# Kernel tuning notes

Hardware: AMD Instinct MI355X
Metric: run time of the kernel (lower is better)

Reference implementation:

```python
import jax, jax.numpy as jnp
import numpy as np

B, L, DIM, H = 2, 2048, 1024, 16
HD = DIM // H  # head dim = 64
MASK_SCALE = -10 * 6  # faithful to the original source: mask_expand *= -10 * 6


def setup_inputs() -> dict:
    key = jax.random.key(0)
    ks = jax.random.split(key, 8)
    s = 1.0 / np.sqrt(DIM)
    return {
        "x": jax.random.normal(ks[0], (B, L, DIM), jnp.float32),
        "attention_mask": jax.random.uniform(ks[1], (B, L, L), jnp.float32),
        "Wq": jax.random.normal(ks[2], (DIM, DIM), jnp.float32) * s,
        "bq": jnp.zeros((DIM,), jnp.float32),
        "Wk": jax.random.normal(ks[3], (DIM, DIM), jnp.float32) * s,
        "bk": jnp.zeros((DIM,), jnp.float32),
        "Wv": jax.random.normal(ks[4], (DIM, DIM), jnp.float32) * s,
        "bv": jnp.zeros((DIM,), jnp.float32),
    }


def _split_heads(t):
    # [B, L, DIM] -> [B, H, L, HD]
    return t.reshape(B, L, H, HD).transpose(0, 2, 1, 3)


def reference(x, attention_mask, Wq, bq, Wk, bk, Wv, bv):
    q = _split_heads(x @ Wq + bq)
    k = _split_heads(x @ Wk + bk)
    v = _split_heads(x @ Wv + bv)
    scale = float(HD) ** -0.5
    # full [B, H, L, L] score matrix, as in the original
    scores = jnp.einsum("bhqd,bhkd->bhqk", q, k) * scale
    scores = scores + attention_mask[:, None, :, :] * MASK_SCALE
    probs = jax.nn.softmax(scores, axis=-1)
    ctx = jnp.einsum("bhqk,bhkd->bhqd", probs, v)
    # merge heads back: [B, L, DIM]
    return ctx.transpose(0, 2, 1, 3).reshape(B, L, DIM)
```

## Files before the change

### kernel.cpp

```cpp
#include <hip/hip_runtime.h>

#define LL 2048
#define NHEADS 16
#define HDIM 64
#define QSCALE 0.18033688011112042f
#define MASKC1 -86.56170245333780f

typedef __attribute__((ext_vector_type(8))) __bf16 bf16x8;
typedef __attribute__((ext_vector_type(4))) float f32x4;

__device__ __forceinline__ unsigned short f2bf(float f) {
  unsigned int u = __builtin_bit_cast(unsigned int, f);
  u += 0x7fffu + ((u >> 16) & 1u);
  return (unsigned short)(u >> 16);
}

__device__ __forceinline__ bf16x8 ld_frag(const unsigned short* p) {
  return *reinterpret_cast<const bf16x8*>(p);
}

__device__ __forceinline__ void async_cp16(const unsigned short* g, unsigned short* l) {
  __builtin_amdgcn_global_load_lds(
      (const __attribute__((address_space(1))) unsigned int*)(unsigned long long)(g),
      (__attribute__((address_space(3))) unsigned int*)(unsigned int)(unsigned long long)(l),
      16, 0, 0);
}

__global__ __launch_bounds__(256) void cvt_x_kernel(const float* __restrict__ x,
                                                    unsigned short* __restrict__ xb) {
  int i = (blockIdx.x * 256 + threadIdx.x) * 4;
  float4 v = *reinterpret_cast<const float4*>(x + i);
  ushort4 o;
  o.x = f2bf(v.x); o.y = f2bf(v.y); o.z = f2bf(v.z); o.w = f2bf(v.w);
  *reinterpret_cast<ushort4*>(xb + i) = o;
}

__global__ __launch_bounds__(256) void transpose_w_kernel(const float* __restrict__ Wq,
                                                          const float* __restrict__ Wk,
                                                          const float* __restrict__ Wv,
                                                          unsigned short* __restrict__ WtAll) {
  int z = blockIdx.z;
  const float* W = (z == 0) ? Wq : (z == 1) ? Wk : Wv;
  unsigned short* dst = WtAll + (size_t)z * 1024 * 1024;
  int n0 = blockIdx.x * 64, k0 = blockIdx.y * 64;
  __shared__ float t[64][65];
  int tx = threadIdx.x & 63, ty = threadIdx.x >> 6;
#pragma unroll
  for (int p = 0; p < 16; ++p) {
    int kr = p * 4 + ty;
    t[kr][tx] = W[(size_t)(k0 + kr) * 1024 + n0 + tx];
  }
  __syncthreads();
#pragma unroll
  for (int p = 0; p < 16; ++p) {
    int nr = p * 4 + ty;
    dst[(size_t)(n0 + nr) * 1024 + k0 + tx] = f2bf(t[tx][nr]);
  }
}

__global__ __launch_bounds__(256) void em_prep_kernel(const float* __restrict__ mask,
                                                      unsigned short* __restrict__ em) {
  int row = blockIdx.y;
  int t = blockIdx.x * 256 + threadIdx.x;
  int kb = t >> 4, c = t & 15;
  const float* src = mask + (size_t)row * LL + kb * 64 + c;
  ushort4 o;
  o.x = f2bf(__builtin_amdgcn_exp2f(src[0]  * MASKC1));
  o.y = f2bf(__builtin_amdgcn_exp2f(src[16] * MASKC1));
  o.z = f2bf(__builtin_amdgcn_exp2f(src[32] * MASKC1));
  o.w = f2bf(__builtin_amdgcn_exp2f(src[48] * MASKC1));
  *reinterpret_cast<ushort4*>(em + (size_t)row * LL + kb * 64 + 4 * c) = o;
}

__global__ __launch_bounds__(256) void qkv_gemm_kernel(
    const unsigned short* __restrict__ xb, const unsigned short* __restrict__ WtAll,
    const float* __restrict__ bq, const float* __restrict__ bk, const float* __restrict__ bv,
    unsigned short* __restrict__ qkv) {
  const int z = blockIdx.z;
  const unsigned short* Wt = WtAll + (size_t)z * 1024 * 1024;
  const float* bias = (z == 0) ? bq : (z == 1) ? bk : bv;
  unsigned short* outb = qkv + (size_t)z * 4194304;

  __shared__ __align__(16) unsigned short smem[16384];
  unsigned short* As = smem;
  unsigned short* Bs = smem + 8192;

  const int tid = threadIdx.x;
  const int w = tid >> 6, lane = tid & 63, g = lane >> 4, cc = lane & 15;
  const int wm = w >> 1, wn = w & 1;
  const int m0 = blockIdx.y * 128, n0 = blockIdx.x * 128;
  const int srow = lane >> 3;
  const int gc = ((lane & 7) - srow) & 7;
  const unsigned short* ga = xb + (size_t)(m0 + w * 32 + srow) * 1024 + gc * 8;
  const unsigned short* gb = Wt + (size_t)(n0 + w * 32 + srow) * 1024 + gc * 8;
  unsigned short* la = As + w * 2048;
  unsigned short* lb = Bs + w * 2048;

  f32x4 acc[4][4];
#pragma unroll
  for (int i = 0; i < 4; ++i)
#pragma unroll
    for (int j = 0; j < 4; ++j) acc[i][j] = (f32x4)0.0f;

  for (int kk = 0; kk < 1024; kk += 64) {
    __syncthreads();
#pragma unroll
    for (int i = 0; i < 4; ++i) {
      async_cp16(ga + i * 8192 + kk, la + i * 512);
      async_cp16(gb + i * 8192 + kk, lb + i * 512);
    }
    __syncthreads();
    bf16x8 af[4][2], bfr[4][2];
#pragma unroll
    for (int mt = 0; mt < 4; ++mt)
#pragma unroll
      for (int ks = 0; ks < 2; ++ks)
        af[mt][ks] = ld_frag(&As[(wm * 64 + mt * 16 + cc) * 64 + ((4 * ks + g + cc) & 7) * 8]);
#pragma unroll
    for (int nt = 0; nt < 4; ++nt)
#pragma unroll
      for (int ks = 0; ks < 2; ++ks)
        bfr[nt][ks] = ld_frag(&Bs[(wn * 64 + nt * 16 + cc) * 64 + ((4 * ks + g + cc) & 7) * 8]);
#pragma unroll
    for (int mt = 0; mt < 4; ++mt)
#pragma unroll
      for (int nt = 0; nt < 4; ++nt)
#pragma unroll
        for (int ks = 0; ks < 2; ++ks)
          acc[mt][nt] = __builtin_amdgcn_mfma_f32_16x16x32_bf16(af[mt][ks], bfr[nt][ks],
                                                                acc[mt][nt], 0, 0, 0);
  }

  if (z != 2) {
    const float sc = (z == 0) ? QSCALE : 1.0f;
#pragma unroll
    for (int nt = 0; nt < 4; ++nt) {
      int n = n0 + wn * 64 + nt * 16 + cc;
      float bval = bias[n];
      int h = n >> 6, d = n & 63;
#pragma unroll
      for (int mt = 0; mt < 4; ++mt) {
#pragma unroll
        for (int r = 0; r < 4; ++r) {
          int m = m0 + wm * 64 + mt * 16 + g * 4 + r;
          int b = m >> 11, l = m & 2047;
          outb[(((size_t)(b * NHEADS + h) * LL) + l) * HDIM + d] =
              f2bf((acc[mt][nt][r] + bval) * sc);
        }
      }
    }
  } else {
    __syncthreads();
#pragma unroll
    for (int nt = 0; nt < 4; ++nt) {
      int nr = wn * 64 + nt * 16 + cc;
      float bval = bias[n0 + nr];
#pragma unroll
      for (int mt = 0; mt < 4; ++mt)
#pragma unroll
        for (int r = 0; r < 4; ++r)
          smem[nr * 128 + wm * 64 + 16 * g + 4 * r + mt] = f2bf(acc[mt][nt][r] + bval);
    }
    __syncthreads();
    int row = tid >> 1, half = tid & 1;
    int n = n0 + row, hh = n >> 6, dd = n & 63;
    int bb = m0 >> 11, l0 = (m0 & 2047) + half * 64;
    unsigned short* dst = outb + ((size_t)(bb * NHEADS + hh) * HDIM + dd) * LL + l0;
#pragma unroll
    for (int i = 0; i < 8; ++i)
      *reinterpret_cast<uint4*>(dst + i * 8) =
          *reinterpret_cast<const uint4*>(&smem[row * 128 + half * 64 + i * 8]);
  }
}

__global__ __launch_bounds__(256) void flash_kernel(
    const unsigned short* __restrict__ Qb, const unsigned short* __restrict__ Kb,
    const unsigned short* __restrict__ Vt, const unsigned short* __restrict__ Em,
    float* __restrict__ out) {
  const int bh = blockIdx.y, b = bh >> 4, h = bh & 15;
  const int q0 = blockIdx.x * 128;
  const int tid = threadIdx.x, w = tid >> 6, lane = tid & 63, g = lane >> 4, cc = lane & 15;
  const size_t bhoff = (size_t)bh * LL * HDIM;

  __shared__ __align__(16) unsigned short Ps[128 * 72];
  __shared__ __align__(16) unsigned short Ks[2][64 * 64];
  __shared__ __align__(16) unsigned short Vs[2][64 * 64];

  bf16x8 aq[2][2];
#pragma unroll
  for (int mt = 0; mt < 2; ++mt)
#pragma unroll
    for (int ks = 0; ks < 2; ++ks)
      aq[mt][ks] = *reinterpret_cast<const bf16x8*>(
          Qb + bhoff + (size_t)(q0 + w * 32 + mt * 16 + cc) * HDIM + ks * 32 + g * 8);

  const int srow = lane >> 3;
  const int gcs = ((lane & 7) - srow) & 7;
  const unsigned short* kg0 = Kb + bhoff + (size_t)(w * 8 + srow) * HDIM + gcs * 8;
  const unsigned short* kg1 = Kb + bhoff + (size_t)(32 + w * 8 + srow) * HDIM + gcs * 8;
  const unsigned short* vg0 = Vt + bhoff + (size_t)(w * 8 + srow) * LL + gcs * 8;
  const unsigned short* vg1 = Vt + bhoff + (size_t)(32 + w * 8 + srow) * LL + gcs * 8;

  float li[2][4];
  f32x4 oacc[2][4];
#pragma unroll
  for (int mt = 0; mt < 2; ++mt) {
#pragma unroll
    for (int r = 0; r < 4; ++r) li[mt][r] = 0.0f;
#pragma unroll
    for (int nt = 0; nt < 4; ++nt) oacc[mt][nt] = (f32x4)0.0f;
  }

  const unsigned short* embase = Em + ((size_t)b * LL + q0 + w * 32) * LL + 4 * cc;

  {
    async_cp16(kg0, Ks[0] + w * 512);
    async_cp16(kg1, Ks[0] + (w + 4) * 512);
    async_cp16(vg0, Vs[0] + w * 512);
    async_cp16(vg1, Vs[0] + (w + 4) * 512);
  }

  for (int kt = 0; kt < 32; ++kt) {
    const int buf = kt & 1;
    __syncthreads();
    if (kt + 1 < 32) {
      const int nb = buf ^ 1;
      async_cp16(kg0 + (size_t)(kt + 1) * 64 * HDIM, Ks[nb] + w * 512);
      async_cp16(kg1 + (size_t)(kt + 1) * 64 * HDIM, Ks[nb] + (w + 4) * 512);
      async_cp16(vg0 + (kt + 1) * 64, Vs[nb] + w * 512);
      async_cp16(vg1 + (kt + 1) * 64, Vs[nb] + (w + 4) * 512);
    }
    uint2 emv[2][4];
#pragma unroll
    for (int mt = 0; mt < 2; ++mt)
#pragma unroll
      for (int r = 0; r < 4; ++r)
        emv[mt][r] = *reinterpret_cast<const uint2*>(
            embase + (size_t)(mt * 16 + g * 4 + r) * LL + kt * 64);

    bf16x8 bk_[4][2];
#pragma unroll
    for (int nt = 0; nt < 4; ++nt)
#pragma unroll
      for (int ks = 0; ks < 2; ++ks)
        bk_[nt][ks] =
            ld_frag(&Ks[buf][(nt * 16 + cc) * 64 + ((4 * ks + g + cc) & 7) * 8]);
    f32x4 sacc[2][4];
#pragma unroll
    for (int mt = 0; mt < 2; ++mt)
#pragma unroll
      for (int nt = 0; nt < 4; ++nt) sacc[mt][nt] = (f32x4)0.0f;
#pragma unroll
    for (int mt = 0; mt < 2; ++mt)
#pragma unroll
      for (int nt = 0; nt < 4; ++nt)
#pragma unroll
        for (int ks = 0; ks < 2; ++ks)
          sacc[mt][nt] = __builtin_amdgcn_mfma_f32_16x16x32_bf16(aq[mt][ks], bk_[nt][ks],
                                                                 sacc[mt][nt], 0, 0, 0);

#pragma unroll
    for (int mt = 0; mt < 2; ++mt) {
#pragma unroll
      for (int r = 0; r < 4; ++r) {
        unsigned int ex = emv[mt][r].x, ey = emv[mt][r].y;
        float e0 = __builtin_bit_cast(float, ex << 16);
        float e1 = __builtin_bit_cast(float, ex & 0xffff0000u);
        float e2 = __builtin_bit_cast(float, ey << 16);
        float e3 = __builtin_bit_cast(float, ey & 0xffff0000u);
        float p0 = __builtin_amdgcn_exp2f(sacc[mt][0][r]) * e0;
        float p1 = __builtin_amdgcn_exp2f(sacc[mt][1][r]) * e1;
        float p2 = __builtin_amdgcn_exp2f(sacc[mt][2][r]) * e2;
        float p3 = __builtin_amdgcn_exp2f(sacc[mt][3][r]) * e3;
        unsigned int u01 = __builtin_amdgcn_perm(__builtin_bit_cast(unsigned int, p1),
                                                 __builtin_bit_cast(unsigned int, p0),
                                                 0x07060302u);
        unsigned int u23 = __builtin_amdgcn_perm(__builtin_bit_cast(unsigned int, p3),
                                                 __builtin_bit_cast(unsigned int, p2),
                                                 0x07060302u);
        li[mt][r] += __builtin_bit_cast(float, u01 << 16) +
                     __builtin_bit_cast(float, u01 & 0xffff0000u) +
                     __builtin_bit_cast(float, u23 << 16) +
                     __builtin_bit_cast(float, u23 & 0xffff0000u);
        uint2 pk; pk.x = u01; pk.y = u23;
        *reinterpret_cast<uint2*>(&Ps[(w * 32 + mt * 16 + g * 4 + r) * 72 + 4 * cc]) = pk;
      }
    }
    asm volatile("" ::: "memory");

    bf16x8 ap[2][2], bv[4][2];
#pragma unroll
    for (int mt = 0; mt < 2; ++mt)
#pragma unroll
      for (int ks = 0; ks < 2; ++ks)
        ap[mt][ks] = ld_frag(&Ps[(w * 32 + mt * 16 + cc) * 72 + ks * 32 + g * 8]);
#pragma unroll
    for (int nt = 0; nt < 4; ++nt)
#pragma unroll
      for (int ks = 0; ks < 2; ++ks)
        bv[nt][ks] =
            ld_frag(&Vs[buf][(nt * 16 + cc) * 64 + ((4 * ks + g + cc) & 7) * 8]);
#pragma unroll
    for (int mt = 0; mt < 2; ++mt)
#pragma unroll
      for (int nt = 0; nt < 4; ++nt)
#pragma unroll
        for (int ks = 0; ks < 2; ++ks)
          oacc[mt][nt] = __builtin_amdgcn_mfma_f32_16x16x32_bf16(ap[mt][ks], bv[nt][ks],
                                                                 oacc[mt][nt], 0, 0, 0);
  }

#pragma unroll
  for (int mt = 0; mt < 2; ++mt)
#pragma unroll
    for (int r = 0; r < 4; ++r) {
      float s = li[mt][r];
      s += __shfl_xor(s, 1);
      s += __shfl_xor(s, 2);
      s += __shfl_xor(s, 4);
      s += __shfl_xor(s, 8);
      float inv = 1.0f / s;
      int qrow = q0 + w * 32 + mt * 16 + g * 4 + r;
#pragma unroll
      for (int nt = 0; nt < 4; ++nt)
        out[((size_t)b * LL + qrow) * 1024 + h * 64 + nt * 16 + cc] = oacc[mt][nt][r] * inv;
    }
}

extern "C" void kernel_launch(void* const* d_in, const int* in_sizes, int n_in,
                              void* d_out, int out_size, void* d_ws, size_t ws_size,
                              hipStream_t stream) {
  const float* x    = (const float*)d_in[0];
  const float* mask = (const float*)d_in[1];
  const float* Wq   = (const float*)d_in[2];
  const float* bq   = (const float*)d_in[3];
  const float* Wk   = (const float*)d_in[4];
  const float* bk   = (const float*)d_in[5];
  const float* Wv   = (const float*)d_in[6];
  const float* bv   = (const float*)d_in[7];
  float* out = (float*)d_out;
  (void)in_sizes; (void)n_in; (void)out_size; (void)ws_size;

  char* ws = (char*)d_ws;
  unsigned short* qkv = (unsigned short*)(ws);
  unsigned short* xb  = (unsigned short*)(ws + (24u << 20));
  unsigned short* Wt  = (unsigned short*)(ws + (32u << 20));
  unsigned short* em  = (unsigned short*)(ws + (24u << 20));

  cvt_x_kernel<<<dim3(4096), dim3(256), 0, stream>>>(x, xb);
  transpose_w_kernel<<<dim3(16, 16, 3), dim3(256), 0, stream>>>(Wq, Wk, Wv, Wt);
  qkv_gemm_kernel<<<dim3(8, 32, 3), dim3(256), 0, stream>>>(xb, Wt, bq, bk, bv, qkv);
  em_prep_kernel<<<dim3(2, 4096), dim3(256), 0, stream>>>(mask, em);
  flash_kernel<<<dim3(16, 32), dim3(256), 0, stream>>>(qkv, qkv + 4194304, qkv + 8388608,
                                                       em, out);
}
```

Measured before the change: 215.9 us.

## Pre-tile log-mask in MFMA fragment layout and seed score accumulators with it

The mask prep now stores the scaled mask in bf16 in log space, laid out per block and thread to match the MFMA accumulator fragment. The flash kernel loads it with two contiguous 16-byte loads and uses it as the initial score accumulator, which removes the per-element multiply by exp(mask). Query tiles shrink from 128 to 64 rows, giving twice as many blocks with a launch-bounds occupancy hint and a remapped block order that groups work for L2 locality. The P tile in LDS now uses an XOR swizzle instead of padding. Rounding the scaled log-mask to bf16 before the exp changes numerics and may add error for large mask values.

```diff
diff --git a/kernel.cpp b/kernel.cpp
--- a/kernel.cpp
+++ b/kernel.cpp
@@ -58,18 +58,26 @@
   }
 }
 
-__global__ __launch_bounds__(256) void em_prep_kernel(const float* __restrict__ mask,
-                                                      unsigned short* __restrict__ em) {
-  int row = blockIdx.y;
-  int t = blockIdx.x * 256 + threadIdx.x;
-  int kb = t >> 4, c = t & 15;
-  const float* src = mask + (size_t)row * LL + kb * 64 + c;
-  ushort4 o;
-  o.x = f2bf(__builtin_amdgcn_exp2f(src[0]  * MASKC1));
-  o.y = f2bf(__builtin_amdgcn_exp2f(src[16] * MASKC1));
-  o.z = f2bf(__builtin_amdgcn_exp2f(src[32] * MASKC1));
-  o.w = f2bf(__builtin_amdgcn_exp2f(src[48] * MASKC1));
-  *reinterpret_cast<ushort4*>(em + (size_t)row * LL + kb * 64 + 4 * c) = o;
+__global__ __launch_bounds__(256) void lem_prep_kernel(const float* __restrict__ mask,
+                                                       unsigned short* __restrict__ lem) {
+  const int qb = blockIdx.x, kt = blockIdx.y, b = blockIdx.z;
+  const int tid = threadIdx.x;
+  const int w = tid >> 6, lane = tid & 63, g = lane >> 4, cc = lane & 15;
+  const float* src = mask + ((size_t)b * LL + qb * 64 + w * 16 + g * 4) * LL + kt * 64 + cc;
+  unsigned int u[8];
+#pragma unroll
+  for (int nt = 0; nt < 4; ++nt) {
+    unsigned short h0 = f2bf(src[0 * LL + nt * 16] * MASKC1);
+    unsigned short h1 = f2bf(src[1 * LL + nt * 16] * MASKC1);
+    unsigned short h2 = f2bf(src[2 * LL + nt * 16] * MASKC1);
+    unsigned short h3 = f2bf(src[3 * LL + nt * 16] * MASKC1);
+    u[nt * 2]     = (unsigned int)h0 | ((unsigned int)h1 << 16);
+    u[nt * 2 + 1] = (unsigned int)h2 | ((unsigned int)h3 << 16);
+  }
+  uint4* dst = reinterpret_cast<uint4*>(
+      lem + ((((size_t)b * 32 + qb) * 32 + kt) * 256 + tid) * 16);
+  dst[0] = make_uint4(u[0], u[1], u[2], u[3]);
+  dst[1] = make_uint4(u[4], u[5], u[6], u[7]);
 }
 
 __global__ __launch_bounds__(256) void qkv_gemm_kernel(
@@ -173,26 +181,27 @@
   }
 }
 
-__global__ __launch_bounds__(256) void flash_kernel(
+__global__ __launch_bounds__(256, 4) void flash_kernel(
     const unsigned short* __restrict__ Qb, const unsigned short* __restrict__ Kb,
-    const unsigned short* __restrict__ Vt, const unsigned short* __restrict__ Em,
+    const unsigned short* __restrict__ Vt, const unsigned short* __restrict__ Lem,
     float* __restrict__ out) {
-  const int bh = blockIdx.y, b = bh >> 4, h = bh & 15;
-  const int q0 = blockIdx.x * 128;
+  const int id = blockIdx.y * 32 + blockIdx.x;
+  const int nid = (id & 7) * 128 + (id >> 3);
+  const int qb = nid & 31, bh = nid >> 5;
+  const int b = bh >> 4, h = bh & 15;
+  const int q0 = qb * 64;
   const int tid = threadIdx.x, w = tid >> 6, lane = tid & 63, g = lane >> 4, cc = lane & 15;
   const size_t bhoff = (size_t)bh * LL * HDIM;
 
-  __shared__ __align__(16) unsigned short Ps[128 * 72];
+  __shared__ __align__(16) unsigned short Ps[64 * 64];
   __shared__ __align__(16) unsigned short Ks[2][64 * 64];
   __shared__ __align__(16) unsigned short Vs[2][64 * 64];
 
-  bf16x8 aq[2][2];
-#pragma unroll
-  for (int mt = 0; mt < 2; ++mt)
-#pragma unroll
-    for (int ks = 0; ks < 2; ++ks)
-      aq[mt][ks] = *reinterpret_cast<const bf16x8*>(
-          Qb + bhoff + (size_t)(q0 + w * 32 + mt * 16 + cc) * HDIM + ks * 32 + g * 8);
+  bf16x8 aq[2];
+#pragma unroll
+  for (int ks = 0; ks < 2; ++ks)
+    aq[ks] = *reinterpret_cast<const bf16x8*>(
+        Qb + bhoff + (size_t)(q0 + w * 16 + cc) * HDIM + ks * 32 + g * 8);
 
   const int srow = lane >> 3;
   const int gcs = ((lane & 7) - srow) & 7;
@@ -201,17 +210,15 @@
   const unsigned short* vg0 = Vt + bhoff + (size_t)(w * 8 + srow) * LL + gcs * 8;
   const unsigned short* vg1 = Vt + bhoff + (size_t)(32 + w * 8 + srow) * LL + gcs * 8;
 
-  float li[2][4];
-  f32x4 oacc[2][4];
-#pragma unroll
-  for (int mt = 0; mt < 2; ++mt) {
-#pragma unroll
-    for (int r = 0; r < 4; ++r) li[mt][r] = 0.0f;
-#pragma unroll
-    for (int nt = 0; nt < 4; ++nt) oacc[mt][nt] = (f32x4)0.0f;
-  }
-
-  const unsigned short* embase = Em + ((size_t)b * LL + q0 + w * 32) * LL + 4 * cc;
+  const uint4* lemp = reinterpret_cast<const uint4*>(
+      Lem + ((((size_t)b * 32 + qb) * 32 + 0) * 256 + tid) * 16);
+
+  float li[4];
+  f32x4 oacc[4];
+#pragma unroll
+  for (int r = 0; r < 4; ++r) li[r] = 0.0f;
+#pragma unroll
+  for (int nt = 0; nt < 4; ++nt) oacc[nt] = (f32x4)0.0f;
 
   {
     async_cp16(kg0, Ks[0] + w * 512);
@@ -230,13 +237,32 @@
       async_cp16(vg0 + (kt + 1) * 64, Vs[nb] + w * 512);
       async_cp16(vg1 + (kt + 1) * 64, Vs[nb] + (w + 4) * 512);
     }
-    uint2 emv[2][4];
-#pragma unroll
-    for (int mt = 0; mt < 2; ++mt)
-#pragma unroll
-      for (int r = 0; r < 4; ++r)
-        emv[mt][r] = *reinterpret_cast<const uint2*>(
-            embase + (size_t)(mt * 16 + g * 4 + r) * LL + kt * 64);
+    uint4 e0 = lemp[0], e1 = lemp[1];
+    lemp += 512;
+    f32x4 sacc[4];
+    {
+      unsigned int ux, uy;
+      ux = e0.x; uy = e0.y;
+      sacc[0][0] = __builtin_bit_cast(float, ux << 16);
+      sacc[0][1] = __builtin_bit_cast(float, ux & 0xffff0000u);
+      sacc[0][2] = __builtin_bit_cast(float, uy << 16);
+      sacc[0][3] = __builtin_bit_cast(float, uy & 0xffff0000u);
+      ux = e0.z; uy = e0.w;
+      sacc[1][0] = __builtin_bit_cast(float, ux << 16);
+      sacc[1][1] = __builtin_bit_cast(float, ux & 0xffff0000u);
+      sacc[1][2] = __builtin_bit_cast(float, uy << 16);
+      sacc[1][3] = __builtin_bit_cast(float, uy & 0xffff0000u);
+      ux = e1.x; uy = e1.y;
+      sacc[2][0] = __builtin_bit_cast(float, ux << 16);
+      sacc[2][1] = __builtin_bit_cast(float, ux & 0xffff0000u);
+      sacc[2][2] = __builtin_bit_cast(float, uy << 16);
+      sacc[2][3] = __builtin_bit_cast(float, uy & 0xffff0000u);
+      ux = e1.z; uy = e1.w;
+      sacc[3][0] = __builtin_bit_cast(float, ux << 16);
+      sacc[3][1] = __builtin_bit_cast(float, ux & 0xffff0000u);
+      sacc[3][2] = __builtin_bit_cast(float, uy << 16);
+      sacc[3][3] = __builtin_bit_cast(float, uy & 0xffff0000u);
+    }
 
     bf16x8 bk_[4][2];
 #pragma unroll
@@ -245,55 +271,40 @@
       for (int ks = 0; ks < 2; ++ks)
         bk_[nt][ks] =
             ld_frag(&Ks[buf][(nt * 16 + cc) * 64 + ((4 * ks + g + cc) & 7) * 8]);
-    f32x4 sacc[2][4];
-#pragma unroll
-    for (int mt = 0; mt < 2; ++mt)
-#pragma unroll
-      for (int nt = 0; nt < 4; ++nt) sacc[mt][nt] = (f32x4)0.0f;
-#pragma unroll
-    for (int mt = 0; mt < 2; ++mt)
-#pragma unroll
-      for (int nt = 0; nt < 4; ++nt)
-#pragma unroll
-        for (int ks = 0; ks < 2; ++ks)
-          sacc[mt][nt] = __builtin_amdgcn_mfma_f32_16x16x32_bf16(aq[mt][ks], bk_[nt][ks],
-                                                                 sacc[mt][nt], 0, 0, 0);
-
-#pragma unroll
-    for (int mt = 0; mt < 2; ++mt) {
-#pragma unroll
-      for (int r = 0; r < 4; ++r) {
-        unsigned int ex = emv[mt][r].x, ey = emv[mt][r].y;
-        float e0 = __builtin_bit_cast(float, ex << 16);
-        float e1 = __builtin_bit_cast(float, ex & 0xffff0000u);
-        float e2 = __builtin_bit_cast(float, ey << 16);
-        float e3 = __builtin_bit_cast(float, ey & 0xffff0000u);
-        float p0 = __builtin_amdgcn_exp2f(sacc[mt][0][r]) * e0;
-        float p1 = __builtin_amdgcn_exp2f(sacc[mt][1][r]) * e1;
-        float p2 = __builtin_amdgcn_exp2f(sacc[mt][2][r]) * e2;
-        float p3 = __builtin_amdgcn_exp2f(sacc[mt][3][r]) * e3;
-        unsigned int u01 = __builtin_amdgcn_perm(__builtin_bit_cast(unsigned int, p1),
-                                                 __builtin_bit_cast(unsigned int, p0),
-                                                 0x07060302u);
-        unsigned int u23 = __builtin_amdgcn_perm(__builtin_bit_cast(unsigned int, p3),
-                                                 __builtin_bit_cast(unsigned int, p2),
-                                                 0x07060302u);
-        li[mt][r] += __builtin_bit_cast(float, u01 << 16) +
-                     __builtin_bit_cast(float, u01 & 0xffff0000u) +
-                     __builtin_bit_cast(float, u23 << 16) +
-                     __builtin_bit_cast(float, u23 & 0xffff0000u);
-        uint2 pk; pk.x = u01; pk.y = u23;
-        *reinterpret_cast<uint2*>(&Ps[(w * 32 + mt * 16 + g * 4 + r) * 72 + 4 * cc]) = pk;
-      }
+#pragma unroll
+    for (int nt = 0; nt < 4; ++nt)
+#pragma unroll
+      for (int ks = 0; ks < 2; ++ks)
+        sacc[nt] = __builtin_amdgcn_mfma_f32_16x16x32_bf16(aq[ks], bk_[nt][ks],
+                                                           sacc[nt], 0, 0, 0);
+
+#pragma unroll
+    for (int r = 0; r < 4; ++r) {
+      float p0 = __builtin_amdgcn_exp2f(sacc[0][r]);
+      float p1 = __builtin_amdgcn_exp2f(sacc[1][r]);
+      float p2 = __builtin_amdgcn_exp2f(sacc[2][r]);
+      float p3 = __builtin_amdgcn_exp2f(sacc[3][r]);
+      unsigned int u01 = __builtin_amdgcn_perm(__builtin_bit_cast(unsigned int, p1),
+                                               __builtin_bit_cast(unsigned int, p0),
+                                               0x07060302u);
+      unsigned int u23 = __builtin_amdgcn_perm(__builtin_bit_cast(unsigned int, p3),
+                                               __builtin_bit_cast(unsigned int, p2),
+                                               0x07060302u);
+      li[r] += __builtin_bit_cast(float, u01 << 16) +
+               __builtin_bit_cast(float, u01 & 0xffff0000u) +
+               __builtin_bit_cast(float, u23 << 16) +
+               __builtin_bit_cast(float, u23 & 0xffff0000u);
+      const int row = w * 16 + g * 4 + r;
+      const int sidx = row * 64 + (((cc >> 1) ^ (row & 7)) << 3) + ((cc & 1) << 2);
+      uint2 pk; pk.x = u01; pk.y = u23;
+      *reinterpret_cast<uint2*>(&Ps[sidx]) = pk;
     }
     asm volatile("" ::: "memory");
 
-    bf16x8 ap[2][2], bv[4][2];
-#pragma unroll
-    for (int mt = 0; mt < 2; ++mt)
-#pragma unroll
-      for (int ks = 0; ks < 2; ++ks)
-        ap[mt][ks] = ld_frag(&Ps[(w * 32 + mt * 16 + cc) * 72 + ks * 32 + g * 8]);
+    bf16x8 ap[2], bv[4][2];
+#pragma unroll
+    for (int ks = 0; ks < 2; ++ks)
+      ap[ks] = ld_frag(&Ps[(w * 16 + cc) * 64 + (((ks * 4 + g) ^ (cc & 7)) << 3)]);
 #pragma unroll
     for (int nt = 0; nt < 4; ++nt)
 #pragma unroll
@@ -301,30 +312,26 @@
         bv[nt][ks] =
             ld_frag(&Vs[buf][(nt * 16 + cc) * 64 + ((4 * ks + g + cc) & 7) * 8]);
 #pragma unroll
-    for (int mt = 0; mt < 2; ++mt)
-#pragma unroll
-      for (int nt = 0; nt < 4; ++nt)
-#pragma unroll
-        for (int ks = 0; ks < 2; ++ks)
-          oacc[mt][nt] = __builtin_amdgcn_mfma_f32_16x16x32_bf16(ap[mt][ks], bv[nt][ks],
-                                                                 oacc[mt][nt], 0, 0, 0);
-  }
-
-#pragma unroll
-  for (int mt = 0; mt < 2; ++mt)
-#pragma unroll
-    for (int r = 0; r < 4; ++r) {
-      float s = li[mt][r];
-      s += __shfl_xor(s, 1);
-      s += __shfl_xor(s, 2);
-      s += __shfl_xor(s, 4);
-      s += __shfl_xor(s, 8);
-      float inv = 1.0f / s;
-      int qrow = q0 + w * 32 + mt * 16 + g * 4 + r;
-#pragma unroll
-      for (int nt = 0; nt < 4; ++nt)
-        out[((size_t)b * LL + qrow) * 1024 + h * 64 + nt * 16 + cc] = oacc[mt][nt][r] * inv;
-    }
+    for (int nt = 0; nt < 4; ++nt)
+#pragma unroll
+      for (int ks = 0; ks < 2; ++ks)
+        oacc[nt] = __builtin_amdgcn_mfma_f32_16x16x32_bf16(ap[ks], bv[nt][ks],
+                                                           oacc[nt], 0, 0, 0);
+  }
+
+#pragma unroll
+  for (int r = 0; r < 4; ++r) {
+    float s = li[r];
+    s += __shfl_xor(s, 1);
+    s += __shfl_xor(s, 2);
+    s += __shfl_xor(s, 4);
+    s += __shfl_xor(s, 8);
+    float inv = 1.0f / s;
+    int qrow = q0 + w * 16 + g * 4 + r;
+#pragma unroll
+    for (int nt = 0; nt < 4; ++nt)
+      out[((size_t)b * LL + qrow) * 1024 + h * 64 + nt * 16 + cc] = oacc[nt][r] * inv;
+  }
 }
 
 extern "C" void kernel_launch(void* const* d_in, const int* in_sizes, int n_in,
@@ -345,12 +352,12 @@
   unsigned short* qkv = (unsigned short*)(ws);
   unsigned short* xb  = (unsigned short*)(ws + (24u << 20));
   unsigned short* Wt  = (unsigned short*)(ws + (32u << 20));
-  unsigned short* em  = (unsigned short*)(ws + (24u << 20));
+  unsigned short* lem = (unsigned short*)(ws + (24u << 20));
 
   cvt_x_kernel<<<dim3(4096), dim3(256), 0, stream>>>(x, xb);
   transpose_w_kernel<<<dim3(16, 16, 3), dim3(256), 0, stream>>>(Wq, Wk, Wv, Wt);
   qkv_gemm_kernel<<<dim3(8, 32, 3), dim3(256), 0, stream>>>(xb, Wt, bq, bk, bv, qkv);
-  em_prep_kernel<<<dim3(2, 4096), dim3(256), 0, stream>>>(mask, em);
-  flash_kernel<<<dim3(16, 32), dim3(256), 0, stream>>>(qkv, qkv + 4194304, qkv + 8388608,
-                                                       em, out);
-}
+  lem_prep_kernel<<<dim3(32, 32, 2), dim3(256), 0, stream>>>(mask, lem);
+  flash_kernel<<<dim3(32, 32), dim3(256), 0, stream>>>(qkv, qkv + 4194304, qkv + 8388608,
+                                                       lem, out);
+}
```

Measured after the change: 219.6 us. Within noise of the previous version (+1.7%).

## Fold log-mask into MFMA accumulator init and keep P in registers

Applied to the files above, without the earlier changes.

The mask prep kernel now writes the scaled log-mask (not exp of it) in a per-thread fragment-ordered layout, so the flash kernel loads it with contiguous uint4 reads and uses it as the initial value of the score accumulator. The QK^T MFMA is computed transposed (K as A operand), so the exponentiated probabilities land directly in the register layout needed as the A operand of the PV MFMA. That removes the LDS round-trip for P and the per-element mask multiply. The V-transpose store layout in the QKV GEMM is permuted to match the new P key ordering. Blocks are also remapped across heads and occupancy is hinted at two blocks per SIMD; bf16 rounding of the log-mask and a larger prep layout are the trade-offs.

```diff
diff --git a/kernel.cpp b/kernel.cpp
--- a/kernel.cpp
+++ b/kernel.cpp
@@ -8,6 +8,7 @@
 
 typedef __attribute__((ext_vector_type(8))) __bf16 bf16x8;
 typedef __attribute__((ext_vector_type(4))) float f32x4;
+typedef __attribute__((ext_vector_type(4))) unsigned int u32x4;
 
 __device__ __forceinline__ unsigned short f2bf(float f) {
   unsigned int u = __builtin_bit_cast(unsigned int, f);
@@ -17,6 +18,17 @@
 
 __device__ __forceinline__ bf16x8 ld_frag(const unsigned short* p) {
   return *reinterpret_cast<const bf16x8*>(p);
+}
+
+__device__ __forceinline__ float bflo(unsigned int u) {
+  return __builtin_bit_cast(float, u << 16);
+}
+__device__ __forceinline__ float bfhi(unsigned int u) {
+  return __builtin_bit_cast(float, u & 0xffff0000u);
+}
+__device__ __forceinline__ unsigned int pack2(float hi, float lo) {
+  return __builtin_amdgcn_perm(__builtin_bit_cast(unsigned int, hi),
+                               __builtin_bit_cast(unsigned int, lo), 0x07060302u);
 }
 
 __device__ __forceinline__ void async_cp16(const unsigned short* g, unsigned short* l) {
@@ -58,18 +70,43 @@
   }
 }
 
-__global__ __launch_bounds__(256) void em_prep_kernel(const float* __restrict__ mask,
-                                                      unsigned short* __restrict__ em) {
-  int row = blockIdx.y;
-  int t = blockIdx.x * 256 + threadIdx.x;
-  int kb = t >> 4, c = t & 15;
-  const float* src = mask + (size_t)row * LL + kb * 64 + c;
-  ushort4 o;
-  o.x = f2bf(__builtin_amdgcn_exp2f(src[0]  * MASKC1));
-  o.y = f2bf(__builtin_amdgcn_exp2f(src[16] * MASKC1));
-  o.z = f2bf(__builtin_amdgcn_exp2f(src[32] * MASKC1));
-  o.w = f2bf(__builtin_amdgcn_exp2f(src[48] * MASKC1));
-  *reinterpret_cast<ushort4*>(em + (size_t)row * LL + kb * 64 + 4 * c) = o;
+__global__ __launch_bounds__(256) void lem_prep_kernel(const float* __restrict__ mask,
+                                                       unsigned short* __restrict__ lem) {
+  const int qb = blockIdx.x, kt = blockIdx.y, b = blockIdx.z;
+  const int tid = threadIdx.x;
+  __shared__ unsigned short lds[128 * 72];
+  {
+    const int r0 = tid >> 4;
+    const int c0 = (tid & 15) * 4;
+#pragma unroll
+    for (int p = 0; p < 8; ++p) {
+      int row = p * 16 + r0;
+      float4 v = *reinterpret_cast<const float4*>(
+          mask + ((size_t)b * LL + qb * 128 + row) * LL + kt * 64 + c0);
+      ushort4 o;
+      o.x = f2bf(v.x * MASKC1); o.y = f2bf(v.y * MASKC1);
+      o.z = f2bf(v.z * MASKC1); o.w = f2bf(v.w * MASKC1);
+      *reinterpret_cast<ushort4*>(&lds[row * 72 + c0]) = o;
+    }
+  }
+  __syncthreads();
+  const int w = tid >> 6, lane = tid & 63, g = lane >> 4, cc = lane & 15;
+  unsigned int ow[16];
+#pragma unroll
+  for (int mt = 0; mt < 2; ++mt) {
+    const int q = w * 32 + mt * 16 + cc;
+#pragma unroll
+    for (int nt = 0; nt < 4; ++nt) {
+      uint2 v = *reinterpret_cast<const uint2*>(&lds[q * 72 + nt * 16 + g * 4]);
+      ow[mt * 8 + nt * 2]     = v.x;
+      ow[mt * 8 + nt * 2 + 1] = v.y;
+    }
+  }
+  uint4* dst = reinterpret_cast<uint4*>(
+      lem + ((((size_t)b * 16 + qb) * 32 + kt) * 256 + tid) * 32);
+#pragma unroll
+  for (int j = 0; j < 4; ++j)
+    dst[j] = make_uint4(ow[4 * j], ow[4 * j + 1], ow[4 * j + 2], ow[4 * j + 3]);
 }
 
 __global__ __launch_bounds__(256) void qkv_gemm_kernel(
@@ -159,7 +196,8 @@
       for (int mt = 0; mt < 4; ++mt)
 #pragma unroll
         for (int r = 0; r < 4; ++r)
-          smem[nr * 128 + wm * 64 + 16 * g + 4 * r + mt] = f2bf(acc[mt][nt][r] + bval);
+          smem[nr * 128 + wm * 64 + (mt >> 1) * 32 + g * 8 + (mt & 1) * 4 + r] =
+              f2bf(acc[mt][nt][r] + bval);
     }
     __syncthreads();
     int row = tid >> 1, half = tid & 1;
@@ -173,16 +211,18 @@
   }
 }
 
-__global__ __launch_bounds__(256) void flash_kernel(
+__global__ __launch_bounds__(256, 2) void flash_kernel(
     const unsigned short* __restrict__ Qb, const unsigned short* __restrict__ Kb,
-    const unsigned short* __restrict__ Vt, const unsigned short* __restrict__ Em,
+    const unsigned short* __restrict__ Vt, const unsigned short* __restrict__ Lem,
     float* __restrict__ out) {
-  const int bh = blockIdx.y, b = bh >> 4, h = bh & 15;
-  const int q0 = blockIdx.x * 128;
+  const int id = blockIdx.y * 16 + blockIdx.x;
+  const int nid = (id & 7) * 64 + (id >> 3);
+  const int qb = nid & 15, bh = nid >> 4;
+  const int b = bh >> 4, h = bh & 15;
+  const int q0 = qb * 128;
   const int tid = threadIdx.x, w = tid >> 6, lane = tid & 63, g = lane >> 4, cc = lane & 15;
   const size_t bhoff = (size_t)bh * LL * HDIM;
 
-  __shared__ __align__(16) unsigned short Ps[128 * 72];
   __shared__ __align__(16) unsigned short Ks[2][64 * 64];
   __shared__ __align__(16) unsigned short Vs[2][64 * 64];
 
@@ -201,17 +241,15 @@
   const unsigned short* vg0 = Vt + bhoff + (size_t)(w * 8 + srow) * LL + gcs * 8;
   const unsigned short* vg1 = Vt + bhoff + (size_t)(32 + w * 8 + srow) * LL + gcs * 8;
 
-  float li[2][4];
+  const uint4* lemp = reinterpret_cast<const uint4*>(
+      Lem + (((size_t)b * 16 + qb) * 32 * 256 + tid) * 32);
+
+  float li[2] = {0.0f, 0.0f};
   f32x4 oacc[2][4];
 #pragma unroll
-  for (int mt = 0; mt < 2; ++mt) {
-#pragma unroll
-    for (int r = 0; r < 4; ++r) li[mt][r] = 0.0f;
+  for (int mt = 0; mt < 2; ++mt)
 #pragma unroll
     for (int nt = 0; nt < 4; ++nt) oacc[mt][nt] = (f32x4)0.0f;
-  }
-
-  const unsigned short* embase = Em + ((size_t)b * LL + q0 + w * 32) * LL + 4 * cc;
 
   {
     async_cp16(kg0, Ks[0] + w * 512);
@@ -230,13 +268,8 @@
       async_cp16(vg0 + (kt + 1) * 64, Vs[nb] + w * 512);
       async_cp16(vg1 + (kt + 1) * 64, Vs[nb] + (w + 4) * 512);
     }
-    uint2 emv[2][4];
-#pragma unroll
-    for (int mt = 0; mt < 2; ++mt)
-#pragma unroll
-      for (int r = 0; r < 4; ++r)
-        emv[mt][r] = *reinterpret_cast<const uint2*>(
-            embase + (size_t)(mt * 16 + g * 4 + r) * LL + kt * 64);
+    uint4 e0 = lemp[0], e1 = lemp[1], e2 = lemp[2], e3 = lemp[3];
+    lemp += 1024;
 
     bf16x8 bk_[4][2];
 #pragma unroll
@@ -245,61 +278,53 @@
       for (int ks = 0; ks < 2; ++ks)
         bk_[nt][ks] =
             ld_frag(&Ks[buf][(nt * 16 + cc) * 64 + ((4 * ks + g + cc) & 7) * 8]);
-    f32x4 sacc[2][4];
-#pragma unroll
-    for (int mt = 0; mt < 2; ++mt)
-#pragma unroll
-      for (int nt = 0; nt < 4; ++nt) sacc[mt][nt] = (f32x4)0.0f;
-#pragma unroll
-    for (int mt = 0; mt < 2; ++mt)
-#pragma unroll
-      for (int nt = 0; nt < 4; ++nt)
-#pragma unroll
-        for (int ks = 0; ks < 2; ++ks)
-          sacc[mt][nt] = __builtin_amdgcn_mfma_f32_16x16x32_bf16(aq[mt][ks], bk_[nt][ks],
-                                                                 sacc[mt][nt], 0, 0, 0);
-
-#pragma unroll
-    for (int mt = 0; mt < 2; ++mt) {
-#pragma unroll
-      for (int r = 0; r < 4; ++r) {
-        unsigned int ex = emv[mt][r].x, ey = emv[mt][r].y;
-        float e0 = __builtin_bit_cast(float, ex << 16);
-        float e1 = __builtin_bit_cast(float, ex & 0xffff0000u);
-        float e2 = __builtin_bit_cast(float, ey << 16);
-        float e3 = __builtin_bit_cast(float, ey & 0xffff0000u);
-        float p0 = __builtin_amdgcn_exp2f(sacc[mt][0][r]) * e0;
-        float p1 = __builtin_amdgcn_exp2f(sacc[mt][1][r]) * e1;
-        float p2 = __builtin_amdgcn_exp2f(sacc[mt][2][r]) * e2;
-        float p3 = __builtin_amdgcn_exp2f(sacc[mt][3][r]) * e3;
-        unsigned int u01 = __builtin_amdgcn_perm(__builtin_bit_cast(unsigned int, p1),
-                                                 __builtin_bit_cast(unsigned int, p0),
-                                                 0x07060302u);
-        unsigned int u23 = __builtin_amdgcn_perm(__builtin_bit_cast(unsigned int, p3),
-                                                 __builtin_bit_cast(unsigned int, p2),
-                                                 0x07060302u);
-        li[mt][r] += __builtin_bit_cast(float, u01 << 16) +
-                     __builtin_bit_cast(float, u01 & 0xffff0000u) +
-                     __builtin_bit_cast(float, u23 << 16) +
-                     __builtin_bit_cast(float, u23 & 0xffff0000u);
-        uint2 pk; pk.x = u01; pk.y = u23;
-        *reinterpret_cast<uint2*>(&Ps[(w * 32 + mt * 16 + g * 4 + r) * 72 + 4 * cc]) = pk;
-      }
-    }
-    asm volatile("" ::: "memory");
-
-    bf16x8 ap[2][2], bv[4][2];
-#pragma unroll
-    for (int mt = 0; mt < 2; ++mt)
-#pragma unroll
-      for (int ks = 0; ks < 2; ++ks)
-        ap[mt][ks] = ld_frag(&Ps[(w * 32 + mt * 16 + cc) * 72 + ks * 32 + g * 8]);
+    bf16x8 bv[4][2];
 #pragma unroll
     for (int nt = 0; nt < 4; ++nt)
 #pragma unroll
       for (int ks = 0; ks < 2; ++ks)
         bv[nt][ks] =
             ld_frag(&Vs[buf][(nt * 16 + cc) * 64 + ((4 * ks + g + cc) & 7) * 8]);
+
+    bf16x8 ap[2][2];
+#pragma unroll
+    for (int mt = 0; mt < 2; ++mt) {
+      f32x4 sacc[4];
+      const uint4 ea = (mt == 0) ? e0 : e2;
+      const uint4 eb = (mt == 0) ? e1 : e3;
+      sacc[0][0] = bflo(ea.x); sacc[0][1] = bfhi(ea.x);
+      sacc[0][2] = bflo(ea.y); sacc[0][3] = bfhi(ea.y);
+      sacc[1][0] = bflo(ea.z); sacc[1][1] = bfhi(ea.z);
+      sacc[1][2] = bflo(ea.w); sacc[1][3] = bfhi(ea.w);
+      sacc[2][0] = bflo(eb.x); sacc[2][1] = bfhi(eb.x);
+      sacc[2][2] = bflo(eb.y); sacc[2][3] = bfhi(eb.y);
+      sacc[3][0] = bflo(eb.z); sacc[3][1] = bfhi(eb.z);
+      sacc[3][2] = bflo(eb.w); sacc[3][3] = bfhi(eb.w);
+#pragma unroll
+      for (int nt = 0; nt < 4; ++nt)
+#pragma unroll
+        for (int ks = 0; ks < 2; ++ks)
+          sacc[nt] = __builtin_amdgcn_mfma_f32_16x16x32_bf16(bk_[nt][ks], aq[mt][ks],
+                                                             sacc[nt], 0, 0, 0);
+      float p[4][4];
+#pragma unroll
+      for (int nt = 0; nt < 4; ++nt)
+#pragma unroll
+        for (int r = 0; r < 4; ++r) p[nt][r] = __builtin_amdgcn_exp2f(sacc[nt][r]);
+      unsigned int wd[8];
+#pragma unroll
+      for (int ks = 0; ks < 2; ++ks) {
+        wd[ks * 4 + 0] = pack2(p[2 * ks][1],     p[2 * ks][0]);
+        wd[ks * 4 + 1] = pack2(p[2 * ks][3],     p[2 * ks][2]);
+        wd[ks * 4 + 2] = pack2(p[2 * ks + 1][1], p[2 * ks + 1][0]);
+        wd[ks * 4 + 3] = pack2(p[2 * ks + 1][3], p[2 * ks + 1][2]);
+        u32x4 uv = {wd[ks * 4], wd[ks * 4 + 1], wd[ks * 4 + 2], wd[ks * 4 + 3]};
+        ap[mt][ks] = __builtin_bit_cast(bf16x8, uv);
+      }
+#pragma unroll
+      for (int j = 0; j < 8; ++j) li[mt] += bflo(wd[j]) + bfhi(wd[j]);
+    }
+
 #pragma unroll
     for (int mt = 0; mt < 2; ++mt)
 #pragma unroll
@@ -311,20 +336,20 @@
   }
 
 #pragma unroll
-  for (int mt = 0; mt < 2; ++mt)
+  for (int mt = 0; mt < 2; ++mt) {
+    float s = li[mt];
+    s += __shfl_xor(s, 16);
+    s += __shfl_xor(s, 32);
 #pragma unroll
     for (int r = 0; r < 4; ++r) {
-      float s = li[mt][r];
-      s += __shfl_xor(s, 1);
-      s += __shfl_xor(s, 2);
-      s += __shfl_xor(s, 4);
-      s += __shfl_xor(s, 8);
-      float inv = 1.0f / s;
+      float sv = __shfl(s, g * 4 + r);
+      float inv = 1.0f / sv;
       int qrow = q0 + w * 32 + mt * 16 + g * 4 + r;
 #pragma unroll
       for (int nt = 0; nt < 4; ++nt)
         out[((size_t)b * LL + qrow) * 1024 + h * 64 + nt * 16 + cc] = oacc[mt][nt][r] * inv;
     }
+  }
 }
 
 extern "C" void kernel_launch(void* const* d_in, const int* in_sizes, int n_in,
@@ -345,12 +370,12 @@
   unsigned short* qkv = (unsigned short*)(ws);
   unsigned short* xb  = (unsigned short*)(ws + (24u << 20));
   unsigned short* Wt  = (unsigned short*)(ws + (32u << 20));
-  unsigned short* em  = (unsigned short*)(ws + (24u << 20));
+  unsigned short* lem = (unsigned short*)(ws + (24u << 20));
 
   cvt_x_kernel<<<dim3(4096), dim3(256), 0, stream>>>(x, xb);
   transpose_w_kernel<<<dim3(16, 16, 3), dim3(256), 0, stream>>>(Wq, Wk, Wv, Wt);
   qkv_gemm_kernel<<<dim3(8, 32, 3), dim3(256), 0, stream>>>(xb, Wt, bq, bk, bv, qkv);
-  em_prep_kernel<<<dim3(2, 4096), dim3(256), 0, stream>>>(mask, em);
+  lem_prep_kernel<<<dim3(16, 32, 2), dim3(256), 0, stream>>>(mask, lem);
   flash_kernel<<<dim3(16, 32), dim3(256), 0, stream>>>(qkv, qkv + 4194304, qkv + 8388608,
-                                                       em, out);
-}
+                                                       lem, out);
+}
```

Result: faster. 208.1 us (-3.6%).
